# Performance work log

Measured on AMD Instinct MI355X. Metric: run time of the kernel, lower is better.

## Reference

```python
import jax, jax.numpy as jnp
import numpy as np
from jax import lax

WIN_SIZE = 11
WIN_SIGMA = 1.5
LEVELS = 5


def _gauss_win(size, sigma):
    coords = jnp.arange(size, dtype=jnp.float32) - size // 2
    g = jnp.exp(-(coords * coords) / (2.0 * sigma * sigma))
    return g / jnp.sum(g)


def _gaussian_filter(x, win):
    # separable depthwise gaussian blur, VALID padding (as in pytorch-msssim)
    C = x.shape[1]
    kh = jnp.tile(win.reshape(1, 1, -1, 1), (C, 1, 1, 1))  # (C,1,K,1)
    kw = jnp.tile(win.reshape(1, 1, 1, -1), (C, 1, 1, 1))  # (C,1,1,K)
    dn = ('NCHW', 'OIHW', 'NCHW')
    x = lax.conv_general_dilated(x, kh, (1, 1), 'VALID', feature_group_count=C, dimension_numbers=dn)
    x = lax.conv_general_dilated(x, kw, (1, 1), 'VALID', feature_group_count=C, dimension_numbers=dn)
    return x


def _ssim(X, Y, win, data_range=1.0):
    K1, K2 = 0.01, 0.03
    C1 = (K1 * data_range) ** 2
    C2 = (K2 * data_range) ** 2
    mu1 = _gaussian_filter(X, win)
    mu2 = _gaussian_filter(Y, win)
    mu1_sq = mu1 * mu1
    mu2_sq = mu2 * mu2
    mu12 = mu1 * mu2
    sigma1_sq = _gaussian_filter(X * X, win) - mu1_sq
    sigma2_sq = _gaussian_filter(Y * Y, win) - mu2_sq
    sigma12 = _gaussian_filter(X * Y, win) - mu12
    cs_map = (2.0 * sigma12 + C2) / (sigma1_sq + sigma2_sq + C2)
    ssim_map = ((2.0 * mu12 + C1) / (mu1_sq + mu2_sq + C1)) * cs_map
    return ssim_map.mean(axis=(2, 3)), cs_map.mean(axis=(2, 3))  # (N,C) each


def _avg_pool2(x):
    # kernel 2, stride 2, count_include_pad=True, pad if odd (matches F.avg_pool2d usage)
    N, C, H, W = x.shape
    ph, pw = H % 2, W % 2
    if ph or pw:
        x = jnp.pad(x, ((0, 0), (0, 0), (ph, ph), (pw, pw)))
    s = lax.reduce_window(x, 0.0, lax.add, (1, 1, 2, 2), (1, 1, 2, 2), 'VALID')
    return s * 0.25


def _ms_ssim(X, Y):
    win = _gauss_win(WIN_SIZE, WIN_SIGMA).astype(X.dtype)
    weights = jnp.array([0.0448, 0.2856, 0.3001, 0.2363, 0.1333], dtype=X.dtype)
    mcs = []
    for i in range(LEVELS):
        ssim_pc, cs = _ssim(X, Y, win, data_range=1.0)
        if i < LEVELS - 1:
            mcs.append(jax.nn.relu(cs))
            X = _avg_pool2(X)
            Y = _avg_pool2(Y)
    vals = jnp.stack(mcs + [jax.nn.relu(ssim_pc)])  # (L, N, C)
    ms = jnp.prod(vals ** weights[:, None, None], axis=0)  # (N, C)
    return jnp.mean(ms)  # size_average=True


def setup_inputs() -> dict:
    key = jax.random.key(0)
    k1, k2 = jax.random.split(key)
    output = jax.random.uniform(k1, (32, 3, 512, 512), dtype=jnp.float32)
    target = jax.random.uniform(k2, (32, 3, 512, 512), dtype=jnp.float32)
    return {"output": output, "target": target}


def reference(output, target):
    return 1.0 - _ms_ssim(output, target)
```

## Files before the change

kernel.cpp:

```cpp
#include <hip/hip_runtime.h>
#include <math.h>


struct GWin { float w[11]; };

__global__ __launch_bounds__(256)
void ssim_l0_kernel(const float* __restrict__ X, const float* __restrict__ Y,
                    float* __restrict__ p1x, float* __restrict__ p1y,
                    float* __restrict__ p2x, float* __restrict__ p2y,
                    float* __restrict__ p3x, float* __restrict__ p3y,
                    float* __restrict__ p4x, float* __restrict__ p4y,
                    float* __restrict__ accum, GWin gw)
{
    const int S = 512, outS = 502, rps = 64;
    __shared__ float4 ab[2][2][264];

    const int tid = threadIdx.x;
    const int ch  = blockIdx.z;
    const int oy0 = blockIdx.x * rps;
    const int gc  = 2 * tid;

    int rowsOut = outS - oy0; if (rowsOut > rps) rowsOut = rps;
    const int NIT = (rowsOut + 11) >> 1;

    const float* Xc = X + (size_t)ch * S * S;
    const float* Yc = Y + (size_t)ch * S * S;

    float2 sx0, sy0, sx1, sy1;

    auto issue = [&](int baseRow) {
        int gr0 = baseRow;     if (gr0 > S - 1) gr0 = S - 1;
        int gr1 = baseRow + 1; if (gr1 > S - 1) gr1 = S - 1;
        sx0 = *reinterpret_cast<const float2*>(Xc + (size_t)gr0 * S + gc);
        sy0 = *reinterpret_cast<const float2*>(Yc + (size_t)gr0 * S + gc);
        sx1 = *reinterpret_cast<const float2*>(Xc + (size_t)gr1 * S + gc);
        sy1 = *reinterpret_cast<const float2*>(Yc + (size_t)gr1 * S + gc);
    };
    auto write_slot = [&](int sl) {
        ab[sl][0][tid] = make_float4(sx0.x + sy0.x, sx0.x - sy0.x,
                                     sx0.y + sy0.y, sx0.y - sy0.y);
        ab[sl][1][tid] = make_float4(sx1.x + sy1.x, sx1.x - sy1.x,
                                     sx1.y + sy1.y, sx1.y - sy1.y);
    };

    float pendP[2][12], pendQ[2][12], pendU[2][12], pendV[2][12];
    #pragma unroll
    for (int c = 0; c < 2; ++c)
        #pragma unroll
        for (int j = 0; j < 12; ++j) { pendP[c][j] = 0.f; pendQ[c][j] = 0.f; pendU[c][j] = 0.f; pendV[c][j] = 0.f; }

    float ssum = 0.f, csum = 0.f;
    const float C1x2 = 2e-4f, C2x2 = 1.8e-3f;
    const bool ok0 = gc < outS, ok1 = (gc + 1) < outS;

    float c1a = 0.f, c1b = 0.f, c2a = 0.f, c2b = 0.f, c3a = 0.f, c3b = 0.f;

    if (tid < 8) {
        float4 z = make_float4(0.f, 0.f, 0.f, 0.f);
        ab[0][0][256 + tid] = z; ab[0][1][256 + tid] = z;
        ab[1][0][256 + tid] = z; ab[1][1][256 + tid] = z;
    }
    issue(oy0);
    write_slot(0);
    issue(oy0 + 2);
    __syncthreads();

    for (int k = 0; k < NIT; ++k) {
        const int sl = k & 1;

        float hP[2][2], hQ[2][2], hU[2][2], hV[2][2];
        float4 u0save[2];
        #pragma unroll
        for (int r = 0; r < 2; ++r) {
            const float4* bp = &ab[sl][r][tid];
            float4 u[6];
            #pragma unroll
            for (int i = 0; i < 6; ++i) u[i] = bp[i];
            u0save[r] = u[0];
            const float* v = reinterpret_cast<const float*>(u);
            float sqa[12], sqb[12];
            #pragma unroll
            for (int j = 0; j < 12; ++j) {
                float a = v[2 * j], b = v[2 * j + 1];
                sqa[j] = a * a; sqb[j] = b * b;
            }
            float P0 = 0.f, Q0 = 0.f, U0 = 0.f, V0 = 0.f;
            float P1 = 0.f, Q1 = 0.f, U1 = 0.f, V1 = 0.f;
            #pragma unroll
            for (int t = 0; t < 11; ++t) {
                float wt = gw.w[t];
                P0 = fmaf(wt, v[2 * t],     P0);
                Q0 = fmaf(wt, v[2 * t + 1], Q0);
                U0 = fmaf(wt, sqa[t],       U0);
                V0 = fmaf(wt, sqb[t],       V0);
                P1 = fmaf(wt, v[2 * t + 2], P1);
                Q1 = fmaf(wt, v[2 * t + 3], Q1);
                U1 = fmaf(wt, sqa[t + 1],   U1);
                V1 = fmaf(wt, sqb[t + 1],   V1);
            }
            hP[r][0] = P0; hQ[r][0] = Q0; hU[r][0] = U0; hV[r][0] = V0;
            hP[r][1] = P1; hQ[r][1] = Q1; hU[r][1] = U1; hV[r][1] = V1;
        }

        #pragma unroll
        for (int c = 0; c < 2; ++c) {
            #pragma unroll
            for (int j = 0; j <= 10; ++j) {
                float wt = gw.w[10 - j];
                pendP[c][j] = fmaf(wt, hP[0][c], pendP[c][j]);
                pendQ[c][j] = fmaf(wt, hQ[0][c], pendQ[c][j]);
                pendU[c][j] = fmaf(wt, hU[0][c], pendU[c][j]);
                pendV[c][j] = fmaf(wt, hV[0][c], pendV[c][j]);
            }
            #pragma unroll
            for (int j = 1; j <= 11; ++j) {
                float wt = gw.w[11 - j];
                pendP[c][j] = fmaf(wt, hP[1][c], pendP[c][j]);
                pendQ[c][j] = fmaf(wt, hQ[1][c], pendQ[c][j]);
                pendU[c][j] = fmaf(wt, hU[1][c], pendU[c][j]);
                pendV[c][j] = fmaf(wt, hV[1][c], pendV[c][j]);
            }
        }

        #pragma unroll
        for (int e = 0; e < 2; ++e) {
            int rel = 2 * k - 10 + e;
            bool rowok = (unsigned)rel < (unsigned)rowsOut;
            #pragma unroll
            for (int c = 0; c < 2; ++c) {
                float p = pendP[c][e], q = pendQ[c][e];
                float uu = pendU[c][e], vv = pendV[c][e];
                float p2 = p * p, q2 = q * q;
                float A = p2 - q2;
                float csn = (uu - vv - A) + C2x2;
                float csd = (uu + vv - p2 - q2) + C2x2;
                float cs  = csn * __builtin_amdgcn_rcpf(csd);
                float ss  = (A + C1x2) * __builtin_amdgcn_rcpf(p2 + q2 + C1x2) * cs;
                if (rowok && (c ? ok1 : ok0)) { ssum += ss; csum += cs; }
            }
        }

        #pragma unroll
        for (int c = 0; c < 2; ++c) {
            #pragma unroll
            for (int j = 0; j < 10; ++j) {
                pendP[c][j] = pendP[c][j + 2]; pendQ[c][j] = pendQ[c][j + 2];
                pendU[c][j] = pendU[c][j + 2]; pendV[c][j] = pendV[c][j + 2];
            }
            pendP[c][10] = 0.f; pendP[c][11] = 0.f;
            pendQ[c][10] = 0.f; pendQ[c][11] = 0.f;
            pendU[c][10] = 0.f; pendU[c][11] = 0.f;
            pendV[c][10] = 0.f; pendV[c][11] = 0.f;
        }

        if (k < 32) {
            float p1a = 0.25f * (u0save[0].x + u0save[0].z + u0save[1].x + u0save[1].z);
            float p1b = 0.25f * (u0save[0].y + u0save[0].w + u0save[1].y + u0save[1].w);
            {
                int prow = (oy0 >> 1) + k;
                size_t o = (size_t)ch * 256 * 256 + (size_t)prow * 256 + tid;
                p1x[o] = 0.5f * (p1a + p1b);
                p1y[o] = 0.5f * (p1a - p1b);
            }
            if ((k & 1) == 0) { c1a = p1a; c1b = p1b; }
            else {
                float ta = c1a + p1a, tb = c1b + p1b;
                float p2a = 0.25f * (ta + __shfl_xor(ta, 1));
                float p2b = 0.25f * (tb + __shfl_xor(tb, 1));
                if ((tid & 1) == 0) {
                    int r2 = (oy0 >> 2) + (k >> 1);
                    size_t o = (size_t)ch * 128 * 128 + (size_t)r2 * 128 + (tid >> 1);
                    p2x[o] = 0.5f * (p2a + p2b);
                    p2y[o] = 0.5f * (p2a - p2b);
                }
                if (((k >> 1) & 1) == 0) { c2a = p2a; c2b = p2b; }
                else {
                    float t3a = c2a + p2a, t3b = c2b + p2b;
                    float p3a = 0.25f * (t3a + __shfl_xor(t3a, 2));
                    float p3b = 0.25f * (t3b + __shfl_xor(t3b, 2));
                    if ((tid & 3) == 0) {
                        int r3 = (oy0 >> 3) + (k >> 2);
                        size_t o = (size_t)ch * 64 * 64 + (size_t)r3 * 64 + (tid >> 2);
                        p3x[o] = 0.5f * (p3a + p3b);
                        p3y[o] = 0.5f * (p3a - p3b);
                    }
                    if (((k >> 2) & 1) == 0) { c3a = p3a; c3b = p3b; }
                    else {
                        float t4a = c3a + p3a, t4b = c3b + p3b;
                        float p4a = 0.25f * (t4a + __shfl_xor(t4a, 4));
                        float p4b = 0.25f * (t4b + __shfl_xor(t4b, 4));
                        if ((tid & 7) == 0) {
                            int r4 = (oy0 >> 4) + (k >> 3);
                            size_t o = (size_t)ch * 32 * 32 + (size_t)r4 * 32 + (tid >> 3);
                            p4x[o] = 0.5f * (p4a + p4b);
                            p4y[o] = 0.5f * (p4a - p4b);
                        }
                    }
                }
            }
        }

        if (k + 1 < NIT) {
            write_slot(sl ^ 1);
            if (k + 2 < NIT) issue(oy0 + 2 * (k + 2));
        }
        __syncthreads();
    }

    for (int off = 32; off > 0; off >>= 1) {
        ssum += __shfl_down(ssum, off);
        csum += __shfl_down(csum, off);
    }
    if ((tid & 63) == 0) {
        atomicAdd(&accum[ch], ssum);
        atomicAdd(&accum[96 + ch], csum);
    }
}

__global__ __launch_bounds__(256)
void ssim_rest_kernel(const float* __restrict__ x1, const float* __restrict__ y1,
                      const float* __restrict__ x2, const float* __restrict__ y2,
                      const float* __restrict__ x3, const float* __restrict__ y3,
                      const float* __restrict__ x4, const float* __restrict__ y4,
                      float* __restrict__ accum, GWin gw)
{
    __shared__ float4 ab[2][2][264];

    const int bid = blockIdx.x;
    const int L = (bid >= 624) ? 3 : (bid >= 576) ? 2 : (bid >= 384) ? 1 : 0;
    const int off0 = (L == 0) ? 0 : (L == 1) ? 384 : (L == 2) ? 576 : 624;
    const int r = bid - off0;

    const int S      = (L == 0) ? 256 : (L == 1) ? 128 : (L == 2) ? 64 : 32;
    const int outS   = (L == 0) ? 246 : (L == 1) ? 118 : (L == 2) ? 54 : 22;
    const int rps    = (L == 0) ? 32  : (L == 1) ? 16  : (L == 2) ? 16 : 22;
    const int tpcLog = (L == 0) ? 7   : (L == 1) ? 6   : (L == 2) ? 5  : 4;
    const int stripsLog = (L == 0) ? 3 : (L == 1) ? 3 : (L == 2) ? 2 : 0;
    const float* Xl = (L == 0) ? x1 : (L == 1) ? x2 : (L == 2) ? x3 : x4;
    const float* Yl = (L == 0) ? y1 : (L == 1) ? y2 : (L == 2) ? y3 : y4;
    float* acc = accum + 192 * (L + 1);

    const int zidx  = r >> stripsLog;
    const int strip = r & ((1 << stripsLog) - 1);

    const int tid = threadIdx.x;
    const int tpc = 1 << tpcLog;
    const int lt  = tid & (tpc - 1);
    const int sub = tid >> tpcLog;
    const int ch  = zidx * (256 >> tpcLog) + sub;
    const int oy0 = strip * rps;
    const int gc  = 2 * lt;

    int rowsOut = outS - oy0; if (rowsOut > rps) rowsOut = rps;
    const int NIT = (rowsOut + 11) >> 1;

    const float* Xc = Xl + (size_t)ch * S * S;
    const float* Yc = Yl + (size_t)ch * S * S;

    float2 sx0, sy0, sx1, sy1;

    auto issue = [&](int baseRow) {
        int gr0 = baseRow;     if (gr0 > S - 1) gr0 = S - 1;
        int gr1 = baseRow + 1; if (gr1 > S - 1) gr1 = S - 1;
        sx0 = *reinterpret_cast<const float2*>(Xc + (size_t)gr0 * S + gc);
        sy0 = *reinterpret_cast<const float2*>(Yc + (size_t)gr0 * S + gc);
        sx1 = *reinterpret_cast<const float2*>(Xc + (size_t)gr1 * S + gc);
        sy1 = *reinterpret_cast<const float2*>(Yc + (size_t)gr1 * S + gc);
    };
    auto write_slot = [&](int sl) {
        ab[sl][0][tid] = make_float4(sx0.x + sy0.x, sx0.x - sy0.x,
                                     sx0.y + sy0.y, sx0.y - sy0.y);
        ab[sl][1][tid] = make_float4(sx1.x + sy1.x, sx1.x - sy1.x,
                                     sx1.y + sy1.y, sx1.y - sy1.y);
    };

    float pendP[2][12], pendQ[2][12], pendU[2][12], pendV[2][12];
    #pragma unroll
    for (int c = 0; c < 2; ++c)
        #pragma unroll
        for (int j = 0; j < 12; ++j) { pendP[c][j] = 0.f; pendQ[c][j] = 0.f; pendU[c][j] = 0.f; pendV[c][j] = 0.f; }

    float ssum = 0.f, csum = 0.f;
    const float C1x2 = 2e-4f, C2x2 = 1.8e-3f;
    const bool ok0 = gc < outS, ok1 = (gc + 1) < outS;

    if (tid < 8) {
        float4 z = make_float4(0.f, 0.f, 0.f, 0.f);
        ab[0][0][256 + tid] = z; ab[0][1][256 + tid] = z;
        ab[1][0][256 + tid] = z; ab[1][1][256 + tid] = z;
    }
    issue(oy0);
    write_slot(0);
    issue(oy0 + 2);
    __syncthreads();

    for (int k = 0; k < NIT; ++k) {
        const int sl = k & 1;

        float hP[2][2], hQ[2][2], hU[2][2], hV[2][2];
        #pragma unroll
        for (int r2 = 0; r2 < 2; ++r2) {
            const float4* bp = &ab[sl][r2][tid];
            float4 u[6];
            #pragma unroll
            for (int i = 0; i < 6; ++i) u[i] = bp[i];
            const float* v = reinterpret_cast<const float*>(u);
            float sqa[12], sqb[12];
            #pragma unroll
            for (int j = 0; j < 12; ++j) {
                float a = v[2 * j], b = v[2 * j + 1];
                sqa[j] = a * a; sqb[j] = b * b;
            }
            float P0 = 0.f, Q0 = 0.f, U0 = 0.f, V0 = 0.f;
            float P1 = 0.f, Q1 = 0.f, U1 = 0.f, V1 = 0.f;
            #pragma unroll
            for (int t = 0; t < 11; ++t) {
                float wt = gw.w[t];
                P0 = fmaf(wt, v[2 * t],     P0);
                Q0 = fmaf(wt, v[2 * t + 1], Q0);
                U0 = fmaf(wt, sqa[t],       U0);
                V0 = fmaf(wt, sqb[t],       V0);
                P1 = fmaf(wt, v[2 * t + 2], P1);
                Q1 = fmaf(wt, v[2 * t + 3], Q1);
                U1 = fmaf(wt, sqa[t + 1],   U1);
                V1 = fmaf(wt, sqb[t + 1],   V1);
            }
            hP[r2][0] = P0; hQ[r2][0] = Q0; hU[r2][0] = U0; hV[r2][0] = V0;
            hP[r2][1] = P1; hQ[r2][1] = Q1; hU[r2][1] = U1; hV[r2][1] = V1;
        }

        #pragma unroll
        for (int c = 0; c < 2; ++c) {
            #pragma unroll
            for (int j = 0; j <= 10; ++j) {
                float wt = gw.w[10 - j];
                pendP[c][j] = fmaf(wt, hP[0][c], pendP[c][j]);
                pendQ[c][j] = fmaf(wt, hQ[0][c], pendQ[c][j]);
                pendU[c][j] = fmaf(wt, hU[0][c], pendU[c][j]);
                pendV[c][j] = fmaf(wt, hV[0][c], pendV[c][j]);
            }
            #pragma unroll
            for (int j = 1; j <= 11; ++j) {
                float wt = gw.w[11 - j];
                pendP[c][j] = fmaf(wt, hP[1][c], pendP[c][j]);
                pendQ[c][j] = fmaf(wt, hQ[1][c], pendQ[c][j]);
                pendU[c][j] = fmaf(wt, hU[1][c], pendU[c][j]);
                pendV[c][j] = fmaf(wt, hV[1][c], pendV[c][j]);
            }
        }

        #pragma unroll
        for (int e = 0; e < 2; ++e) {
            int rel = 2 * k - 10 + e;
            bool rowok = (unsigned)rel < (unsigned)rowsOut;
            #pragma unroll
            for (int c = 0; c < 2; ++c) {
                float p = pendP[c][e], q = pendQ[c][e];
                float uu = pendU[c][e], vv = pendV[c][e];
                float p2 = p * p, q2 = q * q;
                float A = p2 - q2;
                float csn = (uu - vv - A) + C2x2;
                float csd = (uu + vv - p2 - q2) + C2x2;
                float cs  = csn * __builtin_amdgcn_rcpf(csd);
                float ss  = (A + C1x2) * __builtin_amdgcn_rcpf(p2 + q2 + C1x2) * cs;
                if (rowok && (c ? ok1 : ok0)) { ssum += ss; csum += cs; }
            }
        }

        #pragma unroll
        for (int c = 0; c < 2; ++c) {
            #pragma unroll
            for (int j = 0; j < 10; ++j) {
                pendP[c][j] = pendP[c][j + 2]; pendQ[c][j] = pendQ[c][j + 2];
                pendU[c][j] = pendU[c][j + 2]; pendV[c][j] = pendV[c][j + 2];
            }
            pendP[c][10] = 0.f; pendP[c][11] = 0.f;
            pendQ[c][10] = 0.f; pendQ[c][11] = 0.f;
            pendU[c][10] = 0.f; pendU[c][11] = 0.f;
            pendV[c][10] = 0.f; pendV[c][11] = 0.f;
        }

        if (k + 1 < NIT) {
            write_slot(sl ^ 1);
            if (k + 2 < NIT) issue(oy0 + 2 * (k + 2));
        }
        __syncthreads();
    }

    {
        int rw = (tpc < 64) ? tpc : 64;
        for (int off = rw >> 1; off > 0; off >>= 1) {
            ssum += __shfl_down(ssum, off);
            csum += __shfl_down(csum, off);
        }
        if ((lt & 63) == 0) {
            atomicAdd(&acc[ch], ssum);
            atomicAdd(&acc[96 + ch], csum);
        }
    }
}

__global__ void finalize_kernel(const float* __restrict__ accum, float* __restrict__ out)
{
    __shared__ float red[2];
    const int t = threadIdx.x;
    const float w[5]   = {0.0448f, 0.2856f, 0.3001f, 0.2363f, 0.1333f};
    const float inv[5] = {1.f / (502.f * 502.f), 1.f / (246.f * 246.f),
                          1.f / (118.f * 118.f), 1.f / (54.f * 54.f),
                          1.f / (22.f * 22.f)};
    float ms = 0.f;
    if (t < 96) {
        ms = 1.f;
        #pragma unroll
        for (int l = 0; l < 5; ++l) {
            float v = (l < 4) ? accum[l * 192 + 96 + t] : accum[l * 192 + t];
            v *= inv[l];
            v = fmaxf(v, 0.f);
            ms *= powf(v, w[l]);
        }
    }
    for (int off = 32; off > 0; off >>= 1) ms += __shfl_down(ms, off);
    int wid = t >> 6, lane = t & 63;
    if (lane == 0) red[wid] = ms;
    __syncthreads();
    if (t == 0) out[0] = 1.f - (red[0] + red[1]) * (1.f / 96.f);
}

extern "C" void kernel_launch(void* const* d_in, const int* in_sizes, int n_in,
                              void* d_out, int out_size, void* d_ws, size_t ws_size,
                              hipStream_t stream)
{
    (void)in_sizes; (void)n_in; (void)out_size; (void)ws_size;
    const float* X = (const float*)d_in[0];
    const float* Y = (const float*)d_in[1];
    float* out = (float*)d_out;
    float* ws  = (float*)d_ws;

    GWin gw;
    {
        double g[11], s = 0.0;
        for (int i = 0; i < 11; ++i) { double d = i - 5; g[i] = exp(-(d * d) / 4.5); s += g[i]; }
        for (int i = 0; i < 11; ++i) gw.w[i] = (float)(g[i] / s);
    }

    float* accum = ws;
    size_t off = 1024;
    float* p1x = ws + off; off += (size_t)96 * 256 * 256;
    float* p1y = ws + off; off += (size_t)96 * 256 * 256;
    float* p2x = ws + off; off += (size_t)96 * 128 * 128;
    float* p2y = ws + off; off += (size_t)96 * 128 * 128;
    float* p3x = ws + off; off += (size_t)96 * 64 * 64;
    float* p3y = ws + off; off += (size_t)96 * 64 * 64;
    float* p4x = ws + off; off += (size_t)96 * 32 * 32;
    float* p4y = ws + off; off += (size_t)96 * 32 * 32;

    hipMemsetAsync(accum, 0, 5 * 192 * sizeof(float), stream);

    ssim_l0_kernel<<<dim3(8, 1, 96), 256, 0, stream>>>(
        X, Y, p1x, p1y, p2x, p2y, p3x, p3y, p4x, p4y, accum, gw);

    ssim_rest_kernel<<<dim3(630), 256, 0, stream>>>(
        p1x, p1y, p2x, p2y, p3x, p3y, p4x, p4y, accum, gw);

    finalize_kernel<<<1, 128, 0, stream>>>(accum, out);
}
```

Measured before the change: 163.4 us.

## Split deeper pool pyramid out of level-0 SSIM kernel into separate pass

```diff
diff --git a/kernel.cpp b/kernel.cpp
--- a/kernel.cpp
+++ b/kernel.cpp
@@ -5,20 +5,21 @@
 struct GWin { float w[11]; };
 
 __global__ __launch_bounds__(256)
-void ssim_l0_kernel(const float* __restrict__ X, const float* __restrict__ Y,
-                    float* __restrict__ p1x, float* __restrict__ p1y,
-                    float* __restrict__ p2x, float* __restrict__ p2y,
-                    float* __restrict__ p3x, float* __restrict__ p3y,
-                    float* __restrict__ p4x, float* __restrict__ p4y,
-                    float* __restrict__ accum, GWin gw)
+void ssim_rows_kernel(const float* __restrict__ X, const float* __restrict__ Y,
+                      float* __restrict__ poolX, float* __restrict__ poolY,
+                      float* __restrict__ accum,
+                      int S, int outS, int doPool, int rps, int tpcLog, GWin gw)
 {
-    const int S = 512, outS = 502, rps = 64;
     __shared__ float4 ab[2][2][264];
 
     const int tid = threadIdx.x;
-    const int ch  = blockIdx.z;
+    const int tpc = 1 << tpcLog;
+    const int lt  = tid & (tpc - 1);
+    const int sub = tid >> tpcLog;
+    const int ch  = blockIdx.z * (256 >> tpcLog) + sub;
     const int oy0 = blockIdx.x * rps;
-    const int gc  = 2 * tid;
+    const int halfS = S >> 1;
+    const int gc  = 2 * lt;
 
     int rowsOut = outS - oy0; if (rowsOut > rps) rowsOut = rps;
     const int NIT = (rowsOut + 11) >> 1;
@@ -51,9 +52,8 @@
 
     float ssum = 0.f, csum = 0.f;
     const float C1x2 = 2e-4f, C2x2 = 1.8e-3f;
-    const bool ok0 = gc < outS, ok1 = (gc + 1) < outS;
-
-    float c1a = 0.f, c1b = 0.f, c2a = 0.f, c2b = 0.f, c3a = 0.f, c3b = 0.f;
+    const bool ok0 = (gc    ) < outS;
+    const bool ok1 = (gc + 1) < outS;
 
     if (tid < 8) {
         float4 z = make_float4(0.f, 0.f, 0.f, 0.f);
@@ -153,51 +153,13 @@
             pendV[c][10] = 0.f; pendV[c][11] = 0.f;
         }
 
-        if (k < 32) {
-            float p1a = 0.25f * (u0save[0].x + u0save[0].z + u0save[1].x + u0save[1].z);
-            float p1b = 0.25f * (u0save[0].y + u0save[0].w + u0save[1].y + u0save[1].w);
-            {
-                int prow = (oy0 >> 1) + k;
-                size_t o = (size_t)ch * 256 * 256 + (size_t)prow * 256 + tid;
-                p1x[o] = 0.5f * (p1a + p1b);
-                p1y[o] = 0.5f * (p1a - p1b);
-            }
-            if ((k & 1) == 0) { c1a = p1a; c1b = p1b; }
-            else {
-                float ta = c1a + p1a, tb = c1b + p1b;
-                float p2a = 0.25f * (ta + __shfl_xor(ta, 1));
-                float p2b = 0.25f * (tb + __shfl_xor(tb, 1));
-                if ((tid & 1) == 0) {
-                    int r2 = (oy0 >> 2) + (k >> 1);
-                    size_t o = (size_t)ch * 128 * 128 + (size_t)r2 * 128 + (tid >> 1);
-                    p2x[o] = 0.5f * (p2a + p2b);
-                    p2y[o] = 0.5f * (p2a - p2b);
-                }
-                if (((k >> 1) & 1) == 0) { c2a = p2a; c2b = p2b; }
-                else {
-                    float t3a = c2a + p2a, t3b = c2b + p2b;
-                    float p3a = 0.25f * (t3a + __shfl_xor(t3a, 2));
-                    float p3b = 0.25f * (t3b + __shfl_xor(t3b, 2));
-                    if ((tid & 3) == 0) {
-                        int r3 = (oy0 >> 3) + (k >> 2);
-                        size_t o = (size_t)ch * 64 * 64 + (size_t)r3 * 64 + (tid >> 2);
-                        p3x[o] = 0.5f * (p3a + p3b);
-                        p3y[o] = 0.5f * (p3a - p3b);
-                    }
-                    if (((k >> 2) & 1) == 0) { c3a = p3a; c3b = p3b; }
-                    else {
-                        float t4a = c3a + p3a, t4b = c3b + p3b;
-                        float p4a = 0.25f * (t4a + __shfl_xor(t4a, 4));
-                        float p4b = 0.25f * (t4b + __shfl_xor(t4b, 4));
-                        if ((tid & 7) == 0) {
-                            int r4 = (oy0 >> 4) + (k >> 3);
-                            size_t o = (size_t)ch * 32 * 32 + (size_t)r4 * 32 + (tid >> 3);
-                            p4x[o] = 0.5f * (p4a + p4b);
-                            p4y[o] = 0.5f * (p4a - p4b);
-                        }
-                    }
-                }
-            }
+        if (doPool && k < (rps >> 1)) {
+            float sa = u0save[0].x + u0save[0].z + u0save[1].x + u0save[1].z;
+            float sb = u0save[0].y + u0save[0].w + u0save[1].y + u0save[1].w;
+            int prow = (oy0 >> 1) + k;
+            size_t o = (size_t)ch * halfS * halfS + (size_t)prow * halfS + lt;
+            poolX[o] = 0.125f * (sa + sb);
+            poolY[o] = 0.125f * (sa - sb);
         }
 
         if (k + 1 < NIT) {
@@ -207,13 +169,72 @@
         __syncthreads();
     }
 
-    for (int off = 32; off > 0; off >>= 1) {
-        ssum += __shfl_down(ssum, off);
-        csum += __shfl_down(csum, off);
-    }
-    if ((tid & 63) == 0) {
-        atomicAdd(&accum[ch], ssum);
-        atomicAdd(&accum[96 + ch], csum);
+    {
+        int rw = (tpc < 64) ? tpc : 64;
+        for (int off = rw >> 1; off > 0; off >>= 1) {
+            ssum += __shfl_down(ssum, off);
+            csum += __shfl_down(csum, off);
+        }
+        if ((lt & 63) == 0) {
+            atomicAdd(&accum[ch], ssum);
+            atomicAdd(&accum[96 + ch], csum);
+        }
+    }
+}
+
+__global__ __launch_bounds__(256)
+void pool_pyramid_kernel(const float* __restrict__ p1x, const float* __restrict__ p1y,
+                         float* __restrict__ p2x, float* __restrict__ p2y,
+                         float* __restrict__ p3x, float* __restrict__ p3y,
+                         float* __restrict__ p4x, float* __restrict__ p4y)
+{
+    const int tid  = threadIdx.x;
+    const int ch   = blockIdx.y;
+    const int tile = blockIdx.x;
+    const int ty0 = (tile >> 2) * 64, tx0 = (tile & 3) * 64;
+    const int tr = tid >> 4, tc = tid & 15;
+    const int iy = ty0 + 4 * tr, ix = tx0 + 4 * tc;
+
+    const float* X1 = p1x + (size_t)ch * 256 * 256;
+    const float* Y1 = p1y + (size_t)ch * 256 * 256;
+
+    float4 xr[4], yr[4];
+    #pragma unroll
+    for (int r = 0; r < 4; ++r) {
+        xr[r] = *reinterpret_cast<const float4*>(X1 + (size_t)(iy + r) * 256 + ix);
+        yr[r] = *reinterpret_cast<const float4*>(Y1 + (size_t)(iy + r) * 256 + ix);
+    }
+
+    float x200 = 0.25f * (xr[0].x + xr[0].y + xr[1].x + xr[1].y);
+    float x201 = 0.25f * (xr[0].z + xr[0].w + xr[1].z + xr[1].w);
+    float x210 = 0.25f * (xr[2].x + xr[2].y + xr[3].x + xr[3].y);
+    float x211 = 0.25f * (xr[2].z + xr[2].w + xr[3].z + xr[3].w);
+    float y200 = 0.25f * (yr[0].x + yr[0].y + yr[1].x + yr[1].y);
+    float y201 = 0.25f * (yr[0].z + yr[0].w + yr[1].z + yr[1].w);
+    float y210 = 0.25f * (yr[2].x + yr[2].y + yr[3].x + yr[3].y);
+    float y211 = 0.25f * (yr[2].z + yr[2].w + yr[3].z + yr[3].w);
+    {
+        int oy = iy >> 1, ox = ix >> 1;
+        float* bx = p2x + (size_t)ch * 128 * 128;
+        float* by = p2y + (size_t)ch * 128 * 128;
+        *reinterpret_cast<float2*>(bx + (size_t)oy * 128 + ox)       = make_float2(x200, x201);
+        *reinterpret_cast<float2*>(bx + (size_t)(oy + 1) * 128 + ox) = make_float2(x210, x211);
+        *reinterpret_cast<float2*>(by + (size_t)oy * 128 + ox)       = make_float2(y200, y201);
+        *reinterpret_cast<float2*>(by + (size_t)(oy + 1) * 128 + ox) = make_float2(y210, y211);
+    }
+
+    float x3 = 0.25f * (x200 + x201 + x210 + x211);
+    float y3 = 0.25f * (y200 + y201 + y210 + y211);
+    p3x[(size_t)ch * 64 * 64 + (size_t)(iy >> 2) * 64 + (ix >> 2)] = x3;
+    p3y[(size_t)ch * 64 * 64 + (size_t)(iy >> 2) * 64 + (ix >> 2)] = y3;
+
+    float x4 = x3 + __shfl_xor(x3, 1);
+    float y4 = y3 + __shfl_xor(y3, 1);
+    x4 += __shfl_xor(x4, 16);
+    y4 += __shfl_xor(y4, 16);
+    if (((tr | tc) & 1) == 0) {
+        p4x[(size_t)ch * 32 * 32 + (size_t)(iy >> 3) * 32 + (ix >> 3)] = 0.25f * x4;
+        p4y[(size_t)ch * 32 * 32 + (size_t)(iy >> 3) * 32 + (ix >> 3)] = 0.25f * y4;
     }
 }
 
@@ -456,8 +477,11 @@
 
     hipMemsetAsync(accum, 0, 5 * 192 * sizeof(float), stream);
 
-    ssim_l0_kernel<<<dim3(8, 1, 96), 256, 0, stream>>>(
-        X, Y, p1x, p1y, p2x, p2y, p3x, p3y, p4x, p4y, accum, gw);
+    ssim_rows_kernel<<<dim3(8, 1, 96), 256, 0, stream>>>(
+        X, Y, p1x, p1y, accum, 512, 502, 1, 64, 8, gw);
+
+    pool_pyramid_kernel<<<dim3(16, 96), 256, 0, stream>>>(
+        p1x, p1y, p2x, p2y, p3x, p3y, p4x, p4y);
 
     ssim_rest_kernel<<<dim3(630), 256, 0, stream>>>(
         p1x, p1y, p2x, p2y, p3x, p3y, p4x, p4y, accum, gw);
```

After: 150.2 us, median of 2. 1.09x faster.
